# Optimization experiments

Hardware: AMD Instinct MI355X
Metric: run time of the kernel (lower is better)

The kernel has to match this reference:

```python
import jax, jax.numpy as jnp
import numpy as np
import math

T = 4096
HID = 2048
H = 16
D = 128
RD = 64            # rotary_dim = head_dim * partial_rotary_factor (0.5)
THETA = 10000.0
EPS = 1e-6
GROUPS = 8
LAYER_IDX = 2
N_LAYERS = 32


def build_slope_tensor(num_heads):
    def get_slopes_power_of_2(n):
        start = 2 ** (-(2 ** (-(math.log2(n) - 3))))
        ratio = start
        return [start * ratio ** i for i in range(n)]
    if math.log2(num_heads).is_integer():
        return get_slopes_power_of_2(num_heads)
    closest = 2 ** math.floor(math.log2(num_heads))
    return (get_slopes_power_of_2(closest)
            + build_slope_tensor(2 * closest)[0::2][: num_heads - closest])


def compute_slope():
    base = np.array(build_slope_tensor(H), dtype=np.float32)
    return jnp.asarray(-base * (1 - (LAYER_IDX - 1) / (N_LAYERS - 1) + 1e-5), dtype=jnp.float32)


def setup_inputs() -> dict:
    key = jax.random.key(0)
    ks = jax.random.split(key, 8)
    s = 0.02
    return {
        "positions": jnp.arange(T, dtype=jnp.int32),
        "hidden_states": jax.random.normal(ks[0], (T, HID), dtype=jnp.float32),
        "recurrent_state": jnp.zeros((1, H, D, D), dtype=jnp.float32),
        "w_qkv": jax.random.normal(ks[1], (HID, 3 * H * D), dtype=jnp.float32) * s,
        "w_g": jax.random.normal(ks[2], (HID, H * D), dtype=jnp.float32) * s,
        "w_dense": jax.random.normal(ks[3], (H * D, HID), dtype=jnp.float32) * s,
        "q_norm_w": jnp.ones((D,), dtype=jnp.float32),
        "k_norm_w": jnp.ones((D,), dtype=jnp.float32),
        "g_norm_w": jnp.ones((H * D,), dtype=jnp.float32),
    }


def _rms(x, w):
    var = jnp.mean(jnp.square(x), axis=-1, keepdims=True)
    return x * jax.lax.rsqrt(var + EPS) * w


def _rope(x, positions):
    # partial neox-style rotary on first RD dims of each head
    inv_freq = 1.0 / (THETA ** (jnp.arange(0, RD, 2, dtype=jnp.float32) / RD))
    freqs = positions.astype(jnp.float32)[:, None] * inv_freq   # [T, RD/2]
    cos = jnp.cos(freqs)[:, None, :]                            # [T, 1, RD/2]
    sin = jnp.sin(freqs)[:, None, :]
    x1 = x[..., : RD // 2]
    x2 = x[..., RD // 2 : RD]
    x_pass = x[..., RD:]
    return jnp.concatenate([x1 * cos - x2 * sin, x2 * cos + x1 * sin, x_pass], axis=-1)


def reference(positions, hidden_states, recurrent_state,
              w_qkv, w_g, w_dense, q_norm_w, k_norm_w, g_norm_w):
    t = hidden_states.shape[0]
    qkv = (hidden_states @ w_qkv).reshape(t, 3, H, D)
    q, k, v = qkv[:, 0], qkv[:, 1], qkv[:, 2]
    q = _rms(q, q_norm_w)
    k = _rms(k, k_norm_w)
    q = _rope(q, positions)
    k = _rope(k, positions)

    slope = compute_slope()                    # [H], negative
    decay = jnp.exp(slope)                     # per-head per-step decay
    scale = D ** -0.5
    q = (q * scale).astype(jnp.float32)
    k = k.astype(jnp.float32)
    v = v.astype(jnp.float32)

    def step(S, qkv_t):
        q_t, k_t, v_t = qkv_t                  # each [H, D]
        S = S * decay[:, None, None] + k_t[:, :, None] * v_t[:, None, :]
        o_t = jnp.einsum('hk,hkv->hv', q_t, S)
        return S, o_t

    S0 = recurrent_state[0].astype(jnp.float32)   # [H, K, V]
    S_final, o = jax.lax.scan(step, S0, (q, k, v))
    attn = o.reshape(t, H * D)

    gate = jax.nn.sigmoid(hidden_states @ w_g)
    # GroupRMSNorm: normalize per group of size (H*D)/GROUPS, scale by full weight
    g = attn.reshape(t, GROUPS, (H * D) // GROUPS)
    var = jnp.mean(jnp.square(g), axis=-1, keepdims=True)
    g = (g * jax.lax.rsqrt(var + EPS)).reshape(t, H * D) * g_norm_w

    out = (g * gate) @ w_dense
    return out, S_final[None]
```

## Files before the change

### kernel.cpp

```cpp
#include <hip/hip_runtime.h>
#include <hip/hip_bf16.h>

using bf16x8 = __attribute__((ext_vector_type(8))) __bf16;
using f32x4  = __attribute__((ext_vector_type(4))) float;

constexpr int T_SEQ = 4096;
constexpr int HID_C = 2048;
constexpr int NH    = 16;
constexpr int QKV_N = 6144;

__device__ __forceinline__ float head_slope(int h) {
    return -exp2f(-0.5f * (float)(h + 1)) * 0.967751935483871f;
}

__device__ __forceinline__ ushort f2bfu(float f) {
    __hip_bfloat16 h = __float2bfloat16(f);
    return *(ushort*)&h;
}
__device__ __forceinline__ float bfu2f(ushort u) {
    union { unsigned int i; float f; } x; x.i = ((unsigned int)u) << 16; return x.f;
}

__device__ __forceinline__ void async16(const ushort* g, ushort* l) {
    __builtin_amdgcn_global_load_lds((const __attribute__((address_space(1))) void*)g,
                                     (__attribute__((address_space(3))) void*)l, 16, 0, 0);
}

template<int N> __device__ __forceinline__ void waitcnt_vm() {
    if constexpr (N == 0)      asm volatile("s_waitcnt vmcnt(0)" ::: "memory");
    else if constexpr (N == 2) asm volatile("s_waitcnt vmcnt(2)" ::: "memory");
    else if constexpr (N == 4) asm volatile("s_waitcnt vmcnt(4)" ::: "memory");
    else if constexpr (N == 6) asm volatile("s_waitcnt vmcnt(6)" ::: "memory");
}

__device__ __forceinline__ void cvt_body(const float* __restrict__ src, ushort* __restrict__ dst,
                                         int bid, int tid) {
    int i = (bid * 256 + tid) * 8;
    float4 a = *(const float4*)(src + i);
    float4 b = *(const float4*)(src + i + 4);
    ushort4 ua = {f2bfu(a.x), f2bfu(a.y), f2bfu(a.z), f2bfu(a.w)};
    ushort4 ub = {f2bfu(b.x), f2bfu(b.y), f2bfu(b.z), f2bfu(b.w)};
    *(ushort4*)(dst + i) = ua;
    *(ushort4*)(dst + i + 4) = ub;
}

__device__ __forceinline__ void transpose_body(const float* __restrict__ src,
                                               ushort* __restrict__ dst,
                                               int R, int C, int bx, int by, int t,
                                               ushort (*tile)[68]) {
    int tr = by * 64, tc = bx * 64;
    int r0 = t >> 4;
    int c4 = (t & 15) << 2;
#pragma unroll
    for (int p = 0; p < 4; ++p) {
        int row = r0 + p * 16;
        float4 v = *(const float4*)&src[(size_t)(tr + row) * C + tc + c4];
        tile[row][c4 + 0] = f2bfu(v.x);
        tile[row][c4 + 1] = f2bfu(v.y);
        tile[row][c4 + 2] = f2bfu(v.z);
        tile[row][c4 + 3] = f2bfu(v.w);
    }
    __syncthreads();
#pragma unroll
    for (int p = 0; p < 4; ++p) {
        int orow = r0 + p * 16;
        ushort4 u;
        u.x = tile[c4 + 0][orow];
        u.y = tile[c4 + 1][orow];
        u.z = tile[c4 + 2][orow];
        u.w = tile[c4 + 3][orow];
        *(ushort4*)&dst[(size_t)(tc + orow) * R + tr + c4] = u;
    }
}

__global__ __launch_bounds__(256) void prep_all(const float* __restrict__ hidden,
                                                ushort* __restrict__ hid_b,
                                                const float* __restrict__ w_qkv,
                                                ushort* __restrict__ wqkv_t,
                                                const float* __restrict__ w_g,
                                                ushort* __restrict__ wg_t,
                                                const float* __restrict__ w_dense,
                                                ushort* __restrict__ wd_t,
                                                const int* __restrict__ positions,
                                                float2* __restrict__ ropet) {
    __shared__ ushort tile[64][68];
    int b = blockIdx.x, t = threadIdx.x;
    if (b < 4096) {
        cvt_body(hidden, hid_b, b, t);
    } else if (b < 7168) {
        int bb = b - 4096;
        transpose_body(w_qkv, wqkv_t, HID_C, QKV_N, bb % 96, bb / 96, t, tile);
    } else if (b < 8192) {
        int bb = b - 7168;
        transpose_body(w_g, wg_t, HID_C, HID_C, bb % 32, bb / 32, t, tile);
    } else if (b < 9216) {
        int bb = b - 8192;
        transpose_body(w_dense, wd_t, HID_C, HID_C, bb % 32, bb / 32, t, tile);
    } else {
        int i = (b - 9216) * 256 + t;
        int tt = i >> 5, fi = i & 31;
        float inv = expf((float)fi * -0.2878231366f);
        float freq = (float)positions[tt] * inv;
        float sn, cs;
        sincosf(freq, &sn, &cs);
        ropet[i] = make_float2(cs, sn);
    }
}

__device__ __forceinline__ void gemm8w_core(const ushort* __restrict__ Ag,
                                            const ushort* __restrict__ Bg,
                                            int K, int bm, int bn,
                                            ushort* sh, f32x4 (&acc)[4][8]) {
    const int tid  = threadIdx.x;
    const int lane = tid & 63;
    const int wave = tid >> 6;
    const int lane15 = lane & 15, quad = lane >> 4;
    const int wm = wave >> 1, wn = wave & 1;
    const int swz = lane15 & 7;

    ushort* const ldsA0 = sh;
    ushort* const ldsA1 = sh + 16384;
    ushort* const ldsB0 = sh + 32768;
    ushort* const ldsB1 = sh + 49152;

    const int srow = lane >> 3;
    const int scol = ((lane & 7) ^ srow) << 3;
    const ushort* gA = Ag + (size_t)(bm + srow) * K + scol;
    const ushort* gB = Bg + (size_t)(bn + srow) * K + scol;
    const int ro = wave * 16;
    const int NT = K >> 6;

#define STAGE8(L, g, k0) do { \
    _Pragma("unroll") for (int h = 0; h < 2; ++h) \
    _Pragma("unroll") for (int q = 0; q < 2; ++q) \
        async16((g) + (size_t)((h) * 128 + ro + q * 8) * K + (k0), (L) + ((h) * 128 + ro + q * 8) * 64); } while (0)

    STAGE8(ldsA0, gA, 0);
    STAGE8(ldsB0, gB, 0);
    waitcnt_vm<0>();
    asm volatile("s_barrier" ::: "memory");

    for (int t = 0; t < NT; ++t) {
        const ushort* LA = (t & 1) ? ldsA1 : ldsA0;
        const ushort* LB = (t & 1) ? ldsB1 : ldsB0;
        ushort* LAn = (t & 1) ? ldsA0 : ldsA1;
        ushort* LBn = (t & 1) ? ldsB0 : ldsB1;
        bf16x8 af[4][2];
#pragma unroll
        for (int i = 0; i < 4; ++i)
#pragma unroll
            for (int ks = 0; ks < 2; ++ks)
                af[i][ks] = *(const bf16x8*)&LA[(wm * 64 + i * 16 + lane15) * 64 + (((ks * 4 + quad) ^ swz) << 3)];
        bf16x8 bf0[4][2];
#pragma unroll
        for (int j = 0; j < 4; ++j)
#pragma unroll
            for (int ks = 0; ks < 2; ++ks)
                bf0[j][ks] = *(const bf16x8*)&LB[(wn * 128 + j * 16 + lane15) * 64 + (((ks * 4 + quad) ^ swz) << 3)];
        if (t + 1 < NT) {
            STAGE8(LAn, gA, (t + 1) << 6);
            STAGE8(LBn, gB, (t + 1) << 6);
        }
        __builtin_amdgcn_s_setprio(1);
#pragma unroll
        for (int i = 0; i < 4; ++i)
#pragma unroll
            for (int j = 0; j < 4; ++j)
#pragma unroll
                for (int ks = 0; ks < 2; ++ks)
                    acc[i][j] = __builtin_amdgcn_mfma_f32_16x16x32_bf16(af[i][ks], bf0[j][ks], acc[i][j], 0, 0, 0);
        __builtin_amdgcn_s_setprio(0);
        bf16x8 bf1[4][2];
#pragma unroll
        for (int j = 0; j < 4; ++j)
#pragma unroll
            for (int ks = 0; ks < 2; ++ks)
                bf1[j][ks] = *(const bf16x8*)&LB[(wn * 128 + (4 + j) * 16 + lane15) * 64 + (((ks * 4 + quad) ^ swz) << 3)];
        __builtin_amdgcn_s_setprio(1);
#pragma unroll
        for (int i = 0; i < 4; ++i)
#pragma unroll
            for (int j = 0; j < 4; ++j)
#pragma unroll
                for (int ks = 0; ks < 2; ++ks)
                    acc[i][4 + j] = __builtin_amdgcn_mfma_f32_16x16x32_bf16(af[i][ks], bf1[j][ks], acc[i][4 + j], 0, 0, 0);
        __builtin_amdgcn_s_setprio(0);
        waitcnt_vm<0>();
        asm volatile("s_barrier" ::: "memory");
    }
#undef STAGE8
}

__device__ __forceinline__ void gemm4_core(const ushort* __restrict__ Ag,
                                           const ushort* __restrict__ Bg,
                                           int K, int bm, int bn,
                                           ushort* sh, f32x4 (&acc)[4][4]) {
    const int tid  = threadIdx.x;
    const int lane = tid & 63;
    const int wave = tid >> 6;
    const int lane15 = lane & 15, quad = lane >> 4;
    const int wm = wave >> 1, wn = wave & 1;
    const int swz = lane15 & 7;

    ushort* const ldsA0 = sh;
    ushort* const ldsA1 = sh + 8192;
    ushort* const ldsB0 = sh + 16384;
    ushort* const ldsB1 = sh + 24576;

    const int srow = lane >> 3;
    const int scol = ((lane & 7) ^ srow) << 3;
    const ushort* gA = Ag + (size_t)(bm + srow) * K + scol;
    const ushort* gB = Bg + (size_t)(bn + srow) * K + scol;
    const int ro = wave * 32;
    const int NT = K >> 6;

#define STG(L, g, k0) do { \
    _Pragma("unroll") for (int q = 0; q < 4; ++q) \
        async16((g) + (size_t)(ro + q * 8) * K + (k0), (L) + (ro + q * 8) * 64); } while (0)

    STG(ldsA0, gA, 0);
    STG(ldsB0, gB, 0);
    waitcnt_vm<0>();
    asm volatile("s_barrier" ::: "memory");

    for (int t = 0; t < NT; ++t) {
        const ushort* LA = (t & 1) ? ldsA1 : ldsA0;
        const ushort* LB = (t & 1) ? ldsB1 : ldsB0;
        ushort* LAn = (t & 1) ? ldsA0 : ldsA1;
        ushort* LBn = (t & 1) ? ldsB0 : ldsB1;
        bf16x8 bfr[4][2];
#pragma unroll
        for (int j = 0; j < 4; ++j)
#pragma unroll
            for (int ks = 0; ks < 2; ++ks)
                bfr[j][ks] = *(const bf16x8*)&LB[(wn * 64 + j * 16 + lane15) * 64 + (((ks * 4 + quad) ^ swz) << 3)];
        bf16x8 af[4][2];
#pragma unroll
        for (int i = 0; i < 4; ++i)
#pragma unroll
            for (int ks = 0; ks < 2; ++ks)
                af[i][ks] = *(const bf16x8*)&LA[(wm * 64 + i * 16 + lane15) * 64 + (((ks * 4 + quad) ^ swz) << 3)];
        if (t + 1 < NT) {
            STG(LAn, gA, (t + 1) << 6);
            STG(LBn, gB, (t + 1) << 6);
        }
        __builtin_amdgcn_s_setprio(1);
#pragma unroll
        for (int i = 0; i < 4; ++i)
#pragma unroll
            for (int j = 0; j < 4; ++j)
#pragma unroll
                for (int ks = 0; ks < 2; ++ks)
                    acc[i][j] = __builtin_amdgcn_mfma_f32_16x16x32_bf16(af[i][ks], bfr[j][ks], acc[i][j], 0, 0, 0);
        __builtin_amdgcn_s_setprio(0);
        waitcnt_vm<0>();
        asm volatile("s_barrier" ::: "memory");
    }
#undef STG
}

__global__ __launch_bounds__(512, 2) void gemm_fused(const ushort* __restrict__ A,
                                                     const ushort* __restrict__ Bcat,
                                                     ushort* __restrict__ qkv,
                                                     ushort* __restrict__ gate,
                                                     ushort* __restrict__ kT,
                                                     ushort* __restrict__ vT,
                                                     const float2* __restrict__ tab,
                                                     const float* __restrict__ qw,
                                                     const float* __restrict__ kw, int K) {
    __shared__ ushort sh[65536];
    int bid = blockIdx.x;
    int x = bid & 7, w = bid >> 3;
    int rm = x >> 2, rn = x & 3;
    int wm_i = w >> 3, wn_i = w & 7;
    int bm = (rm * 8 + wm_i) * 256;
    int bn = (rn * 8 + wn_i) * 256;
    f32x4 acc[4][8] = {};
    gemm8w_core(A, Bcat, K, bm, bn, sh, acc);

    int lane = threadIdx.x & 63, wave = threadIdx.x >> 6;
    int lane15 = lane & 15, quad = lane >> 4;
    int wm = wave >> 1, wn = wave & 1;
    constexpr int S = 132;

    if (bn < 4096) {
        bool isq = bn < 2048;
        const float* wnorm = isq ? qw : kw;
        float w8a[8];
#pragma unroll
        for (int j = 0; j < 8; ++j) w8a[j] = wnorm[j * 16 + lane15];
        float sc = isq ? 0.08838834764831845f : 1.0f;
        int rowbase = bm + wm * 64;
#pragma unroll
        for (int i = 0; i < 4; ++i)
#pragma unroll
            for (int r = 0; r < 4; ++r) {
                float s2 = 0.f;
#pragma unroll
                for (int j = 0; j < 8; ++j) { float xv = acc[i][j][r]; s2 += xv * xv; }
                s2 += __shfl_xor(s2, 1);
                s2 += __shfl_xor(s2, 2);
                s2 += __shfl_xor(s2, 4);
                s2 += __shfl_xor(s2, 8);
                float rr = rsqrtf(s2 * (1.0f / 128.0f) + 1e-6f);
                float xx[8];
#pragma unroll
                for (int j = 0; j < 8; ++j) xx[j] = acc[i][j][r] * rr * w8a[j];
                int t = rowbase + i * 16 + quad * 4 + r;
                float2 rt0 = tab[t * 32 + lane15];
                float2 rt1 = tab[t * 32 + 16 + lane15];
                float a0 = xx[0], b0 = xx[2], a1 = xx[1], b1 = xx[3];
                xx[0] = a0 * rt0.x - b0 * rt0.y;
                xx[2] = b0 * rt0.x + a0 * rt0.y;
                xx[1] = a1 * rt1.x - b1 * rt1.y;
                xx[3] = b1 * rt1.x + a1 * rt1.y;
#pragma unroll
                for (int j = 0; j < 8; ++j) acc[i][j][r] = xx[j] * sc;
            }
#pragma unroll
        for (int i = 0; i < 4; ++i)
#pragma unroll
            for (int j = 0; j < 8; ++j) {
                int col = bn + wn * 128 + j * 16 + lane15;
#pragma unroll
                for (int r = 0; r < 4; ++r)
                    qkv[(size_t)(rowbase + i * 16 + quad * 4 + r) * QKV_N + col] = f2bfu(acc[i][j][r]);
            }
        if (!isq) {
            ushort* L = sh;
            int h0 = (bn - 2048) >> 7;
            int c0 = bm >> 7;
#pragma unroll
            for (int cq = 0; cq < 2; ++cq) {
                if ((wm >> 1) == cq) {
#pragma unroll
                    for (int i = 0; i < 4; ++i)
#pragma unroll
                        for (int j = 0; j < 8; ++j) {
                            int d_local = j * 16 + lane15;
#pragma unroll
                            for (int r = 0; r < 4; ++r) {
                                int t_local = (wm & 1) * 64 + i * 16 + quad * 4 + r;
                                L[wn * 128 * S + d_local * S + t_local] = f2bfu(acc[i][j][r]);
                            }
                        }
                }
                __syncthreads();
#pragma unroll
                for (int p = 0; p < 16; ++p) {
                    int lin = (p * 512 + threadIdx.x) * 4;
                    int hq2 = lin >> 14;
                    int wi = lin & 16383;
                    int d = wi >> 7, t4 = wi & 127;
                    const ushort* lp = &L[hq2 * 128 * S + d * S + t4];
                    ushort4 u = { lp[0], lp[1], lp[2], lp[3] };
                    *(ushort4*)&kT[((size_t)((h0 + hq2) * 32 + c0 + cq) * 128 + d) * 128 + t4] = u;
                }
                __syncthreads();
            }
        }
        return;
    }

    if (bn < QKV_N) {
        ushort* L = sh;
        int h0 = (bn - 4096) >> 7;
        int c0 = bm >> 7;
#pragma unroll
        for (int cq = 0; cq < 2; ++cq) {
            if ((wm >> 1) == cq) {
#pragma unroll
                for (int i = 0; i < 4; ++i)
#pragma unroll
                    for (int j = 0; j < 8; ++j) {
                        int d_local = j * 16 + lane15;
#pragma unroll
                        for (int r = 0; r < 4; ++r) {
                            int t_local = (wm & 1) * 64 + i * 16 + quad * 4 + r;
                            L[wn * 128 * S + d_local * S + t_local] = f2bfu(acc[i][j][r]);
                        }
                    }
            }
            __syncthreads();
#pragma unroll
            for (int p = 0; p < 16; ++p) {
                int lin = (p * 512 + threadIdx.x) * 4;
                int hq2 = lin >> 14;
                int wi = lin & 16383;
                int d = wi >> 7, t4 = wi & 127;
                const ushort* lp = &L[hq2 * 128 * S + d * S + t4];
                ushort4 u = { lp[0], lp[1], lp[2], lp[3] };
                *(ushort4*)&vT[((size_t)((h0 + hq2) * 32 + c0 + cq) * 128 + d) * 128 + t4] = u;
            }
            __syncthreads();
        }
        return;
    }

    int cb = (bn - QKV_N) + wn * 128;
    int rb = bm + wm * 64;
#pragma unroll
    for (int i = 0; i < 4; ++i)
#pragma unroll
        for (int j = 0; j < 8; ++j) {
            int col = cb + j * 16 + lane15;
#pragma unroll
            for (int r = 0; r < 4; ++r) {
                float v = 1.0f / (1.0f + __expf(-acc[i][j][r]));
                gate[(size_t)(rb + i * 16 + quad * 4 + r) * HID_C + col] = f2bfu(v);
            }
        }
}

__global__ __launch_bounds__(256, 2) void gemm_dense(const ushort* __restrict__ A,
                                                     const ushort* __restrict__ Bt,
                                                     float* __restrict__ Cout, int N, int K) {
    __shared__ ushort sh[32768];
    int bid = blockIdx.x;
    int x = bid & 7, w = bid >> 3;
    int rm = x >> 1, rn = x & 1;
    int wm_i = w >> 3, wn_i = w & 7;
    int bm = (rm * 8 + wm_i) * 128;
    int bn = (rn * 8 + wn_i) * 128;
    f32x4 acc[4][4] = {};
    gemm4_core(A, Bt, K, bm, bn, sh, acc);

    int lane = threadIdx.x & 63, wave = threadIdx.x >> 6;
    int lane15 = lane & 15, quad = lane >> 4;
    int wm = wave >> 1, wn = wave & 1;
    int cb = bn + wn * 64;
    int rb = bm + wm * 64;
#pragma unroll
    for (int i = 0; i < 4; ++i)
#pragma unroll
        for (int j = 0; j < 4; ++j) {
            int col = cb + j * 16 + lane15;
#pragma unroll
            for (int r = 0; r < 4; ++r)
                Cout[(size_t)(rb + i * 16 + quad * 4 + r) * N + col] = acc[i][j][r];
        }
}

__global__ __launch_bounds__(256) void chunk_partial(const ushort* __restrict__ kT,
                                                     const ushort* __restrict__ vT,
                                                     ushort* __restrict__ PT) {
    int c = blockIdx.x, h = blockIdx.y;
    float slope = head_slope(h);
    float lam_inv = __expf(-slope);
    int tid = threadIdx.x, lane = tid & 63, wave = tid >> 6;
    int lane15 = lane & 15, quad = lane >> 4;
    int wv = (wave & 1) * 64, wd = (wave >> 1) * 64;
    const ushort* vbase = vT + ((size_t)(h * 32 + c) * 128) * 128;
    const ushort* kbase = kT + ((size_t)(h * 32 + c) * 128) * 128;
    f32x4 acc[4][4] = {};
#pragma unroll
    for (int j0 = 0; j0 < 128; j0 += 32) {
        float w8[8];
        w8[0] = __expf(slope * (float)(127 - (j0 + quad * 8)));
#pragma unroll
        for (int kk = 1; kk < 8; ++kk) w8[kk] = w8[kk - 1] * lam_inv;
        bf16x8 afr[4], bfr[4];
#pragma unroll
        for (int i = 0; i < 4; ++i) {
            bf16x8 v = *(const bf16x8*)&vbase[(size_t)(wv + i * 16 + lane15) * 128 + j0 + quad * 8];
#pragma unroll
            for (int kk = 0; kk < 8; ++kk) afr[i][kk] = (__bf16)((float)v[kk] * w8[kk]);
        }
#pragma unroll
        for (int j = 0; j < 4; ++j)
            bfr[j] = *(const bf16x8*)&kbase[(size_t)(wd + j * 16 + lane15) * 128 + j0 + quad * 8];
#pragma unroll
        for (int i = 0; i < 4; ++i)
#pragma unroll
            for (int j = 0; j < 4; ++j)
                acc[i][j] = __builtin_amdgcn_mfma_f32_16x16x32_bf16(afr[i], bfr[j], acc[i][j], 0, 0, 0);
    }
    ushort* out = PT + ((size_t)c * 16 + h) * 16384;
#pragma unroll
    for (int i = 0; i < 4; ++i)
#pragma unroll
        for (int j = 0; j < 4; ++j)
#pragma unroll
            for (int r = 0; r < 4; ++r)
                out[(size_t)(wv + i * 16 + quad * 4 + r) * 128 + wd + j * 16 + lane15] = f2bfu(acc[i][j][r]);
}

__global__ __launch_bounds__(128) void scan_states(const ushort* __restrict__ PT,
                                                   const float* __restrict__ S0,
                                                   ushort* __restrict__ Spb,
                                                   float* __restrict__ Sfin) {
    int hv = blockIdx.x;
    int d = threadIdx.x;
    int h = hv >> 7, v = hv & 127;
    float lamC = __expf(head_slope(h) * 128.0f);
    float s = S0[(size_t)h * 16384 + d * 128 + v];
#pragma unroll
    for (int c = 0; c < 32; ++c) {
        size_t idx = ((size_t)c * 2048 + hv) * 128 + d;
        Spb[idx] = f2bfu(s);
        s = s * lamC + bfu2f(PT[idx]);
    }
    Sfin[(size_t)h * 16384 + d * 128 + v] = s;
}

__global__ __launch_bounds__(256) void chunk_out(const ushort* __restrict__ qkv,
                                                 const ushort* __restrict__ vT,
                                                 const ushort* __restrict__ Spb,
                                                 ushort* __restrict__ o) {
    int c = blockIdx.x, h = blockIdx.y;
    float slope = head_slope(h);
    __shared__ ushort Ps[128 * 136];
    int tid = threadIdx.x, lane = tid & 63, wave = tid >> 6;
    int lane15 = lane & 15, quad = lane >> 4;
    int t0 = c * 128;
    int tt0 = wave, tt1 = 7 - wave;
    const ushort* qbase = qkv + (size_t)t0 * QKV_N + h * 128;
    const ushort* kbase = qbase + 2048;

    bf16x8 qf0[4], qf1[4];
#pragma unroll
    for (int ds = 0; ds < 4; ++ds) {
        qf0[ds] = *(const bf16x8*)&qbase[(size_t)(tt0 * 16 + lane15) * QKV_N + ds * 32 + quad * 8];
        qf1[ds] = *(const bf16x8*)&qbase[(size_t)(tt1 * 16 + lane15) * QKV_N + ds * 32 + quad * 8];
    }
    f32x4 s0a[4] = {};
    f32x4 s1a[8] = {};
#pragma unroll
    for (int st = 0; st < 8; ++st) {
        if (st <= tt1) {
            bf16x8 kf[4];
#pragma unroll
            for (int ds = 0; ds < 4; ++ds)
                kf[ds] = *(const bf16x8*)&kbase[(size_t)(st * 16 + lane15) * QKV_N + ds * 32 + quad * 8];
#pragma unroll
            for (int ds = 0; ds < 4; ++ds)
                s1a[st] = __builtin_amdgcn_mfma_f32_16x16x32_bf16(qf1[ds], kf[ds], s1a[st], 0, 0, 0);
            if (st <= tt0) {
#pragma unroll
                for (int ds = 0; ds < 4; ++ds)
                    s0a[st] = __builtin_amdgcn_mfma_f32_16x16x32_bf16(qf0[ds], kf[ds], s0a[st], 0, 0, 0);
            }
        }
    }
    int stmax0 = tt0 + ((tt0 & 1) ? 0 : 1);
    int stmax1 = tt1 + ((tt1 & 1) ? 0 : 1);
#pragma unroll
    for (int st = 0; st < 8; ++st) {
        if (st <= stmax1) {
#pragma unroll
            for (int r = 0; r < 4; ++r) {
                int t = tt1 * 16 + quad * 4 + r;
                int s = st * 16 + lane15;
                float val = 0.f;
                if (st <= tt1) val = (s <= t) ? s1a[st][r] * __expf(slope * (float)(t - s)) : 0.f;
                Ps[t * 136 + s] = f2bfu(val);
            }
        }
    }
#pragma unroll
    for (int st = 0; st < 5; ++st) {
        if (st <= stmax0) {
#pragma unroll
            for (int r = 0; r < 4; ++r) {
                int t = tt0 * 16 + quad * 4 + r;
                int s = st * 16 + lane15;
                float val = 0.f;
                if (st <= tt0) val = (s <= t) ? s0a[st][r] * __expf(slope * (float)(t - s)) : 0.f;
                Ps[t * 136 + s] = f2bfu(val);
            }
        }
    }
    __syncthreads();
    f32x4 oa0[8] = {};
    f32x4 oa1[8] = {};
    float lam0 = __expf(slope * (float)(tt0 * 16 + lane15 + 1));
    float lam1 = __expf(slope * (float)(tt1 * 16 + lane15 + 1));
    bf16x8 qs0[4], qs1[4];
#pragma unroll
    for (int ds = 0; ds < 4; ++ds)
#pragma unroll
        for (int kk = 0; kk < 8; ++kk) {
            qs0[ds][kk] = (__bf16)((float)qf0[ds][kk] * lam0);
            qs1[ds][kk] = (__bf16)((float)qf1[ds][kk] * lam1);
        }
    const ushort* spb = Spb + ((size_t)c * 2048 + h * 128) * 128;
#pragma unroll
    for (int vt = 0; vt < 8; ++vt)
#pragma unroll
        for (int ds = 0; ds < 4; ++ds) {
            bf16x8 bfrag = *(const bf16x8*)&spb[(vt * 16 + lane15) * 128 + ds * 32 + quad * 8];
            oa0[vt] = __builtin_amdgcn_mfma_f32_16x16x32_bf16(qs0[ds], bfrag, oa0[vt], 0, 0, 0);
            oa1[vt] = __builtin_amdgcn_mfma_f32_16x16x32_bf16(qs1[ds], bfrag, oa1[vt], 0, 0, 0);
        }
    const ushort* vbase = vT + ((size_t)(h * 32 + c) * 128) * 128;
    int ns0 = (tt0 + 2) >> 1, ns1 = (tt1 + 2) >> 1;
#pragma unroll
    for (int s32 = 0; s32 < 4; ++s32) {
        if (s32 < ns1) {
            bf16x8 af = *(const bf16x8*)&Ps[(tt1 * 16 + lane15) * 136 + s32 * 32 + quad * 8];
#pragma unroll
            for (int vt = 0; vt < 8; ++vt) {
                bf16x8 bfrag = *(const bf16x8*)&vbase[(size_t)(vt * 16 + lane15) * 128 + s32 * 32 + quad * 8];
                oa1[vt] = __builtin_amdgcn_mfma_f32_16x16x32_bf16(af, bfrag, oa1[vt], 0, 0, 0);
            }
        }
    }
#pragma unroll
    for (int s32 = 0; s32 < 2; ++s32) {
        if (s32 < ns0) {
            bf16x8 af = *(const bf16x8*)&Ps[(tt0 * 16 + lane15) * 136 + s32 * 32 + quad * 8];
#pragma unroll
            for (int vt = 0; vt < 8; ++vt) {
                bf16x8 bfrag = *(const bf16x8*)&vbase[(size_t)(vt * 16 + lane15) * 128 + s32 * 32 + quad * 8];
                oa0[vt] = __builtin_amdgcn_mfma_f32_16x16x32_bf16(af, bfrag, oa0[vt], 0, 0, 0);
            }
        }
    }
#pragma unroll
    for (int vt = 0; vt < 8; ++vt)
#pragma unroll
        for (int r = 0; r < 4; ++r) {
            o[(size_t)(t0 + tt0 * 16 + quad * 4 + r) * 2048 + h * 128 + vt * 16 + lane15] = f2bfu(oa0[vt][r]);
            o[(size_t)(t0 + tt1 * 16 + quad * 4 + r) * 2048 + h * 128 + vt * 16 + lane15] = f2bfu(oa1[vt][r]);
        }
}

__global__ __launch_bounds__(256) void gnorm_gate(const ushort* __restrict__ o,
                                                  const ushort* __restrict__ gate,
                                                  const float* __restrict__ gw,
                                                  ushort* __restrict__ gg) {
    int t = blockIdx.x;
    int tid = threadIdx.x;
    const ushort* op = o + (size_t)t * 2048 + tid * 8;
    bf16x8 xv = *(const bf16x8*)op;
    float x[8];
    float ss = 0.0f;
#pragma unroll
    for (int i = 0; i < 8; ++i) { x[i] = (float)xv[i]; ss += x[i] * x[i]; }
#pragma unroll
    for (int off = 16; off > 0; off >>= 1) ss += __shfl_xor(ss, off);
    float r = rsqrtf(ss * (1.0f / 256.0f) + 1e-6f);
    const ushort* gp = gate + (size_t)t * 2048;
#pragma unroll
    for (int i = 0; i < 8; ++i) {
        int j = tid * 8 + i;
        float val = x[i] * r * gw[j] * bfu2f(gp[j]);
        gg[(size_t)t * 2048 + j] = f2bfu(val);
    }
}

extern "C" void kernel_launch(void* const* d_in, const int* in_sizes, int n_in,
                              void* d_out, int out_size, void* d_ws, size_t ws_size,
                              hipStream_t stream) {
    const int* positions   = (const int*)d_in[0];
    const float* hidden    = (const float*)d_in[1];
    const float* S0        = (const float*)d_in[2];
    const float* w_qkv     = (const float*)d_in[3];
    const float* w_g       = (const float*)d_in[4];
    const float* w_dense   = (const float*)d_in[5];
    const float* qw        = (const float*)d_in[6];
    const float* kw        = (const float*)d_in[7];
    const float* gw        = (const float*)d_in[8];

    char* ws = (char*)d_ws;
    ushort* qkv     = (ushort*)ws;
    ushort* wqkv_t  = (ushort*)(ws + 50331648);
    ushort* wg_t    = (ushort*)(ws + 75497472);
    float2* ropet   = (float2*)(ws + 159383552);
    ushort* PT      = (ushort*)(ws + 50331648);
    ushort* wd_t    = (ushort*)(ws + 83886080);
    ushort* gatebuf = (ushort*)(ws + 92274688);
    ushort* hid_b   = (ushort*)(ws + 109051904);
    ushort* Spb     = (ushort*)(ws + 109051904);
    ushort* kT      = (ushort*)(ws + 125829120);
    ushort* vT      = (ushort*)(ws + 142606336);
    ushort* gg      = (ushort*)ws;

    float* out  = (float*)d_out;
    float* Sfin = out + (size_t)T_SEQ * HID_C;
    ushort* obuf = (ushort*)d_out;

    prep_all<<<9728, 256, 0, stream>>>(hidden, hid_b, w_qkv, wqkv_t, w_g, wg_t,
                                       w_dense, wd_t, positions, ropet);

    gemm_fused<<<dim3(512), 512, 0, stream>>>(hid_b, wqkv_t, qkv, gatebuf, kT, vT,
                                              ropet, qw, kw, HID_C);

    chunk_partial<<<dim3(32, 16), 256, 0, stream>>>(kT, vT, PT);
    scan_states<<<2048, 128, 0, stream>>>(PT, S0, Spb, Sfin);
    chunk_out<<<dim3(32, 16), 256, 0, stream>>>(qkv, vT, Spb, obuf);
    gnorm_gate<<<T_SEQ, 256, 0, stream>>>(obuf, gatebuf, gw, gg);

    gemm_dense<<<dim3(512), 256, 0, stream>>>(gg, wd_t, out, HID_C, HID_C);
}
```

Before: 389.0 us.

## Fuse group RMSNorm and gating into chunk_out, processing two heads per block

The chunk output kernel now handles two heads per 512-thread block, which together form one normalization group of 256 channels. It reduces squared sums across the two heads through shared memory, then applies the group RMSNorm, norm weight and sigmoid gate before writing the gated bf16 result directly. This removes the separate gnorm_gate launch and the round trip of the intermediate attention output through global memory. In exchange the block is larger, uses twice the shared memory and has fewer blocks, and the gg buffer moves to a workspace region that PT previously occupied.

```diff
diff --git a/kernel.cpp b/kernel.cpp
--- a/kernel.cpp
+++ b/kernel.cpp
@@ -503,17 +503,23 @@
     Sfin[(size_t)h * 16384 + d * 128 + v] = s;
 }
 
-__global__ __launch_bounds__(256) void chunk_out(const ushort* __restrict__ qkv,
+__global__ __launch_bounds__(512) void chunk_out(const ushort* __restrict__ qkv,
                                                  const ushort* __restrict__ vT,
                                                  const ushort* __restrict__ Spb,
-                                                 ushort* __restrict__ o) {
-    int c = blockIdx.x, h = blockIdx.y;
-    float slope = head_slope(h);
-    __shared__ ushort Ps[128 * 136];
+                                                 const ushort* __restrict__ gate,
+                                                 const float* __restrict__ gw,
+                                                 ushort* __restrict__ gg) {
+    int c = blockIdx.x, hp = blockIdx.y;
+    __shared__ ushort Ps[2 * 128 * 136];
+    __shared__ float ssb[2 * 128];
     int tid = threadIdx.x, lane = tid & 63, wave = tid >> 6;
     int lane15 = lane & 15, quad = lane >> 4;
+    int hh = wave >> 2, h = hp * 2 + hh;
+    int wv4 = wave & 3;
+    float slope = head_slope(h);
     int t0 = c * 128;
-    int tt0 = wave, tt1 = 7 - wave;
+    int tt0 = wv4, tt1 = 7 - wv4;
+    ushort* PsH = Ps + hh * 128 * 136;
     const ushort* qbase = qkv + (size_t)t0 * QKV_N + h * 128;
     const ushort* kbase = qbase + 2048;
 
@@ -553,7 +559,7 @@
                 int s = st * 16 + lane15;
                 float val = 0.f;
                 if (st <= tt1) val = (s <= t) ? s1a[st][r] * __expf(slope * (float)(t - s)) : 0.f;
-                Ps[t * 136 + s] = f2bfu(val);
+                PsH[t * 136 + s] = f2bfu(val);
             }
         }
     }
@@ -566,7 +572,7 @@
                 int s = st * 16 + lane15;
                 float val = 0.f;
                 if (st <= tt0) val = (s <= t) ? s0a[st][r] * __expf(slope * (float)(t - s)) : 0.f;
-                Ps[t * 136 + s] = f2bfu(val);
+                PsH[t * 136 + s] = f2bfu(val);
             }
         }
     }
@@ -597,7 +603,7 @@
 #pragma unroll
     for (int s32 = 0; s32 < 4; ++s32) {
         if (s32 < ns1) {
-            bf16x8 af = *(const bf16x8*)&Ps[(tt1 * 16 + lane15) * 136 + s32 * 32 + quad * 8];
+            bf16x8 af = *(const bf16x8*)&PsH[(tt1 * 16 + lane15) * 136 + s32 * 32 + quad * 8];
 #pragma unroll
             for (int vt = 0; vt < 8; ++vt) {
                 bf16x8 bfrag = *(const bf16x8*)&vbase[(size_t)(vt * 16 + lane15) * 128 + s32 * 32 + quad * 8];
@@ -608,7 +614,7 @@
 #pragma unroll
     for (int s32 = 0; s32 < 2; ++s32) {
         if (s32 < ns0) {
-            bf16x8 af = *(const bf16x8*)&Ps[(tt0 * 16 + lane15) * 136 + s32 * 32 + quad * 8];
+            bf16x8 af = *(const bf16x8*)&PsH[(tt0 * 16 + lane15) * 136 + s32 * 32 + quad * 8];
 #pragma unroll
             for (int vt = 0; vt < 8; ++vt) {
                 bf16x8 bfrag = *(const bf16x8*)&vbase[(size_t)(vt * 16 + lane15) * 128 + s32 * 32 + quad * 8];
@@ -617,35 +623,43 @@
         }
     }
 #pragma unroll
-    for (int vt = 0; vt < 8; ++vt)
-#pragma unroll
-        for (int r = 0; r < 4; ++r) {
-            o[(size_t)(t0 + tt0 * 16 + quad * 4 + r) * 2048 + h * 128 + vt * 16 + lane15] = f2bfu(oa0[vt][r]);
-            o[(size_t)(t0 + tt1 * 16 + quad * 4 + r) * 2048 + h * 128 + vt * 16 + lane15] = f2bfu(oa1[vt][r]);
-        }
-}
-
-__global__ __launch_bounds__(256) void gnorm_gate(const ushort* __restrict__ o,
-                                                  const ushort* __restrict__ gate,
-                                                  const float* __restrict__ gw,
-                                                  ushort* __restrict__ gg) {
-    int t = blockIdx.x;
-    int tid = threadIdx.x;
-    const ushort* op = o + (size_t)t * 2048 + tid * 8;
-    bf16x8 xv = *(const bf16x8*)op;
-    float x[8];
-    float ss = 0.0f;
-#pragma unroll
-    for (int i = 0; i < 8; ++i) { x[i] = (float)xv[i]; ss += x[i] * x[i]; }
-#pragma unroll
-    for (int off = 16; off > 0; off >>= 1) ss += __shfl_xor(ss, off);
-    float r = rsqrtf(ss * (1.0f / 256.0f) + 1e-6f);
-    const ushort* gp = gate + (size_t)t * 2048;
-#pragma unroll
-    for (int i = 0; i < 8; ++i) {
-        int j = tid * 8 + i;
-        float val = x[i] * r * gw[j] * bfu2f(gp[j]);
-        gg[(size_t)t * 2048 + j] = f2bfu(val);
+    for (int r = 0; r < 4; ++r) {
+        float s20 = 0.f, s21 = 0.f;
+#pragma unroll
+        for (int vt = 0; vt < 8; ++vt) {
+            float a = oa0[vt][r], b = oa1[vt][r];
+            s20 += a * a; s21 += b * b;
+        }
+#pragma unroll
+        for (int m = 1; m <= 8; m <<= 1) {
+            s20 += __shfl_xor(s20, m);
+            s21 += __shfl_xor(s21, m);
+        }
+        if (lane15 == 0) {
+            ssb[hh * 128 + tt0 * 16 + quad * 4 + r] = s20;
+            ssb[hh * 128 + tt1 * 16 + quad * 4 + r] = s21;
+        }
+    }
+    __syncthreads();
+    float gwv[8];
+#pragma unroll
+    for (int vt = 0; vt < 8; ++vt) gwv[vt] = gw[h * 128 + vt * 16 + lane15];
+#pragma unroll
+    for (int r = 0; r < 4; ++r) {
+        int row0 = tt0 * 16 + quad * 4 + r;
+        int row1 = tt1 * 16 + quad * 4 + r;
+        float rr0 = rsqrtf((ssb[row0] + ssb[128 + row0]) * (1.0f / 256.0f) + 1e-6f);
+        float rr1 = rsqrtf((ssb[row1] + ssb[128 + row1]) * (1.0f / 256.0f) + 1e-6f);
+        const ushort* g0 = gate + (size_t)(t0 + row0) * HID_C + h * 128;
+        const ushort* g1 = gate + (size_t)(t0 + row1) * HID_C + h * 128;
+        ushort* o0 = gg + (size_t)(t0 + row0) * HID_C + h * 128;
+        ushort* o1 = gg + (size_t)(t0 + row1) * HID_C + h * 128;
+#pragma unroll
+        for (int vt = 0; vt < 8; ++vt) {
+            int col = vt * 16 + lane15;
+            o0[col] = f2bfu(oa0[vt][r] * rr0 * gwv[vt] * bfu2f(g0[col]));
+            o1[col] = f2bfu(oa1[vt][r] * rr1 * gwv[vt] * bfu2f(g1[col]));
+        }
     }
 }
 
@@ -668,17 +682,16 @@
     ushort* wg_t    = (ushort*)(ws + 75497472);
     float2* ropet   = (float2*)(ws + 159383552);
     ushort* PT      = (ushort*)(ws + 50331648);
+    ushort* gg      = (ushort*)(ws + 50331648);
     ushort* wd_t    = (ushort*)(ws + 83886080);
     ushort* gatebuf = (ushort*)(ws + 92274688);
     ushort* hid_b   = (ushort*)(ws + 109051904);
     ushort* Spb     = (ushort*)(ws + 109051904);
     ushort* kT      = (ushort*)(ws + 125829120);
     ushort* vT      = (ushort*)(ws + 142606336);
-    ushort* gg      = (ushort*)ws;
 
     float* out  = (float*)d_out;
     float* Sfin = out + (size_t)T_SEQ * HID_C;
-    ushort* obuf = (ushort*)d_out;
 
     prep_all<<<9728, 256, 0, stream>>>(hidden, hid_b, w_qkv, wqkv_t, w_g, wg_t,
                                        w_dense, wd_t, positions, ropet);
@@ -688,8 +701,7 @@
 
     chunk_partial<<<dim3(32, 16), 256, 0, stream>>>(kT, vT, PT);
     scan_states<<<2048, 128, 0, stream>>>(PT, S0, Spb, Sfin);
-    chunk_out<<<dim3(32, 16), 256, 0, stream>>>(qkv, vT, Spb, obuf);
-    gnorm_gate<<<T_SEQ, 256, 0, stream>>>(obuf, gatebuf, gw, gg);
+    chunk_out<<<dim3(32, 8), 512, 0, stream>>>(qkv, vT, Spb, gatebuf, gw, gg);
 
     gemm_dense<<<dim3(512), 256, 0, stream>>>(gg, wd_t, out, HID_C, HID_C);
 }
```

Result: faster. 376.8 us (-3.1%).
